# Kernel optimization log

Measured on AMD Instinct MI355X. Metric: run time of the kernel, lower is better.

Reference implementation:

```python
import jax, jax.numpy as jnp
import numpy as np

B, S, H, NH = 8, 4096, 1024, 16
DH = H // NH  # head dim = 64
EPS = 1e-12


def setup_inputs() -> dict:
    key = jax.random.key(0)
    ks = jax.random.split(key, 10)
    sc = 1.0 / np.sqrt(H)
    return {
        "input_tensor": jax.random.normal(ks[0], (B, S, H), dtype=jnp.float32),
        "Wq": jax.random.normal(ks[1], (H, H), dtype=jnp.float32) * sc,
        "bq": jnp.zeros((H,), dtype=jnp.float32),
        "Wk": jax.random.normal(ks[2], (H, H), dtype=jnp.float32) * sc,
        "bk": jnp.zeros((H,), dtype=jnp.float32),
        "Wv": jax.random.normal(ks[3], (H, H), dtype=jnp.float32) * sc,
        "bv": jnp.zeros((H,), dtype=jnp.float32),
        "Wd": jax.random.normal(ks[4], (H, H), dtype=jnp.float32) * sc,
        "bd": jnp.zeros((H,), dtype=jnp.float32),
        "gamma": jnp.ones((H,), dtype=jnp.float32),
        "beta": jnp.zeros((H,), dtype=jnp.float32),
    }


def _heads(x):
    # [B,S,H] -> [B,NH,S,DH]
    return x.reshape(B, S, NH, DH).transpose(0, 2, 1, 3)


def reference(input_tensor, Wq, bq, Wk, bk, Wv, bv, Wd, bd, gamma, beta):
    q = _heads(input_tensor @ Wq + bq)  # [B,NH,S,DH]
    k = _heads(input_tensor @ Wk + bk)
    v = _heads(input_tensor @ Wv + bv)

    eq = jax.nn.elu(q)
    ek = jax.nn.elu(k)
    # L2-normalize per token along the head dim (matches norm over dim=3 of Q
    # and dim=2 of the [B,NH,DH,S]-permuted K in the torch code)
    qn = eq / jnp.linalg.norm(eq, axis=-1, keepdims=True)
    kn = ek / jnp.linalg.norm(ek, axis=-1, keepdims=True)

    kv = jnp.einsum("bhsd,bhse->bhde", kn, v)          # [B,NH,DH,DH]
    ctx = jnp.einsum("bhsd,bhde->bhse", qn, kv) / jnp.sqrt(jnp.float32(DH))
    ctx = ctx.transpose(0, 2, 1, 3).reshape(B, S, H)    # merge heads

    hidden = ctx @ Wd + bd
    x = hidden + input_tensor
    mu = jnp.mean(x, axis=-1, keepdims=True)
    var = jnp.mean(jnp.square(x - mu), axis=-1, keepdims=True)
    return (x - mu) / jnp.sqrt(var + EPS) * gamma + beta
```

## Files before the change

### kernel.cpp

```cpp
#include <hip/hip_runtime.h>
#include <cstdint>
#include <cstddef>

#define B_ 8
#define S_ 4096
#define H_ 1024
#define NH_ 16
#define DH_ 64
#define MTOK 32768

typedef unsigned short u16;
typedef __bf16 bf16x8 __attribute__((ext_vector_type(8)));
typedef u16 u16x8 __attribute__((ext_vector_type(8)));
typedef u16 u16x4 __attribute__((ext_vector_type(4)));
typedef float f32x4 __attribute__((ext_vector_type(4)));

#define DEVFN static __device__ __forceinline__

DEVFN float bf2f(u16 u) {
  union { uint32_t u; float f; } c; c.u = ((uint32_t)u) << 16; return c.f;
}
DEVFN u16 f2bf(float f) {
  union { float f; uint32_t u; } c; c.f = f;
  uint32_t r = c.u + 0x7fffu + ((c.u >> 16) & 1u);
  return (u16)(r >> 16);
}
DEVFN void gload16(const void* g, void* lds_p) {
  __builtin_amdgcn_global_load_lds(
      (const __attribute__((address_space(1))) void*)g,
      (__attribute__((address_space(3))) void*)lds_p, 16, 0, 0);
}

__global__ __launch_bounds__(256) void k_cvt_x(const float* __restrict__ x,
                                               u16* __restrict__ xb) {
  const size_t i = ((size_t)blockIdx.x * 256 + threadIdx.x) * 8;
  f32x4 a = *(const f32x4*)(x + i);
  f32x4 b = *(const f32x4*)(x + i + 4);
  u16x8 o;
#pragma unroll
  for (int j = 0; j < 4; ++j) { o[j] = f2bf(a[j]); o[4 + j] = f2bf(b[j]); }
  *(u16x8*)(xb + i) = o;
}

__global__ __launch_bounds__(256) void k_wt(const float* __restrict__ Wq,
                                            const float* __restrict__ Wk,
                                            const float* __restrict__ Wv,
                                            const float* __restrict__ Wd,
                                            u16* __restrict__ Wt,
                                            u16* __restrict__ Wdt) {
  const int n = blockIdx.x * 256 + threadIdx.x;
  const int kc = blockIdx.y;
  const int g = blockIdx.z;
  const float* W = (g == 0) ? Wq : (g == 1) ? Wk : (g == 2) ? Wv : Wd;
  u16x8 o;
#pragma unroll
  for (int j = 0; j < 8; ++j) o[j] = f2bf(W[(size_t)(kc * 8 + j) * 1024 + n]);
  u16* dst = (g < 3) ? (Wt + ((size_t)(g * 1024 + n)) * 1024 + kc * 8)
                     : (Wdt + (size_t)n * 1024 + kc * 8);
  *(u16x8*)dst = o;
}

template <int EPI>
__global__ __launch_bounds__(512, 2) void k_g(
    const u16* __restrict__ A, const u16* __restrict__ Bt,
    u16* __restrict__ o0, u16* __restrict__ o1, u16* __restrict__ o2,
    const float* __restrict__ b0, const float* __restrict__ b1,
    const float* __restrict__ b2) {
  __shared__ u16 As[2 * 128 * 32];
  __shared__ u16 Bs[2 * 256 * 32];
  const int tid = threadIdx.x;
  const int w = tid >> 6, l = tid & 63;
  const int wm = w >> 2, wn = w & 3;

  const int bid = (int)blockIdx.x;
  const int xcd = bid & 7, c = bid >> 3;
  int bx, by;
  if (EPI == 0) { by = c % 12; bx = xcd * 32 + c / 12; }
  else          { by = c & 3;  bx = xcd * 32 + (c >> 2); }

  const long row0 = (long)bx * 128;
  const long col0 = (long)by * 256;
  const u16* Bt2 = Bt + (EPI == 1 ? ((size_t)(row0 >> 12) << 20) : (size_t)0);

  f32x4 acc[4][4];
#pragma unroll
  for (int i = 0; i < 4; ++i)
#pragma unroll
    for (int j = 0; j < 4; ++j) acc[i][j] = (f32x4){0.f, 0.f, 0.f, 0.f};

  const u16* gA = A + (row0 + (tid >> 2)) * 1024 + (tid & 3) * 8;
  const u16* gB = Bt2 + (col0 + (tid >> 2)) * 1024 + (tid & 3) * 8;
  u16* lA = As + (w * 64) * 8;
  u16* lB = Bs + (w * 64) * 8;

  const int aoff = (wm * 64 + (l & 15)) * 32 + (l >> 4) * 8;
  const int boff = (wn * 64 + (l & 15)) * 32 + (l >> 4) * 8;

  for (int kt = 0; kt < 1024; kt += 64) {
    gload16(gA + kt, lA);
    gload16(gA + kt + 32, lA + 4096);
#pragma unroll
    for (int i = 0; i < 4; ++i) {
      const int go = (i & 1) * 131072 + (i >> 1) * 32 + kt;
      gload16(gB + go, lB + i * 4096);
    }
    __syncthreads();
#pragma unroll
    for (int kh = 0; kh < 2; ++kh) {
      bf16x8 af[4], bfr[4];
#pragma unroll
      for (int mi = 0; mi < 4; ++mi)
        af[mi] = *(const bf16x8*)(As + kh * 4096 + aoff + mi * 512);
#pragma unroll
      for (int ni = 0; ni < 4; ++ni)
        bfr[ni] = *(const bf16x8*)(Bs + kh * 8192 + boff + ni * 512);
#pragma unroll
      for (int mi = 0; mi < 4; ++mi)
#pragma unroll
        for (int ni = 0; ni < 4; ++ni)
          acc[mi][ni] = __builtin_amdgcn_mfma_f32_16x16x32_bf16(
              af[mi], bfr[ni], acc[mi][ni], 0, 0, 0);
    }
    __syncthreads();
  }

  const int rb = (int)row0 + wm * 64 + ((l >> 4) << 2);
  const int cb = (int)col0 + wn * 64 + (l & 15);
  if (EPI == 0) {
    const int seg = (int)(col0 >> 10);
    const int cl = cb & 1023;
    u16* outp = (seg == 0) ? o0 : (seg == 1) ? o1 : o2;
    const float* bias = (seg == 0) ? b0 : (seg == 1) ? b1 : b2;
#pragma unroll
    for (int mi = 0; mi < 4; ++mi)
#pragma unroll
      for (int ni = 0; ni < 4; ++ni) {
        const float bv_ = bias[cl + ni * 16];
#pragma unroll
        for (int r = 0; r < 4; ++r) {
          float v = acc[mi][ni][r] + bv_;
          if (seg < 2) v = v > 0.f ? v : expm1f(v);
          outp[(size_t)(rb + mi * 16 + r) * 1024 + cl + ni * 16] = f2bf(v);
        }
      }
  } else {
#pragma unroll
    for (int mi = 0; mi < 4; ++mi)
#pragma unroll
      for (int ni = 0; ni < 4; ++ni)
#pragma unroll
        for (int r = 0; r < 4; ++r)
          o0[(size_t)(rb + mi * 16 + r) * 1024 + cb + ni * 16] =
              f2bf(acc[mi][ni][r]);
  }
}

__global__ __launch_bounds__(256) void k_qn(u16* __restrict__ eq) {
  const int tid = threadIdx.x, w = tid >> 6, l = tid & 63;
  const long t = (long)blockIdx.x * 4 + w;
  const size_t base = (size_t)t * 1024 + (l >> 2) * 64 + (l & 3) * 16;
  u16x8 a = *(const u16x8*)(eq + base);
  u16x8 b = *(const u16x8*)(eq + base + 8);
  float f[16];
#pragma unroll
  for (int j = 0; j < 8; ++j) { f[j] = bf2f(a[j]); f[8 + j] = bf2f(b[j]); }
  float ss = 0.f;
#pragma unroll
  for (int j = 0; j < 16; ++j) ss += f[j] * f[j];
  ss += __shfl_xor(ss, 1);
  ss += __shfl_xor(ss, 2);
  const float rq = rsqrtf(ss);
  u16x8 oa, ob;
#pragma unroll
  for (int j = 0; j < 8; ++j) { oa[j] = f2bf(f[j] * rq); ob[j] = f2bf(f[8 + j] * rq); }
  *(u16x8*)(eq + base) = oa;
  *(u16x8*)(eq + base + 8) = ob;
}

__global__ __launch_bounds__(256) void k_kv(const u16* __restrict__ ek,
                                            const u16* __restrict__ vv,
                                            float* __restrict__ kvp) {
  __shared__ __align__(16) char lds[69632];
  const int tid = threadIdx.x, w = tid >> 6, l = tid & 63;
  const int bid = blockIdx.x;
  const int sc = bid & 3, h = (bid >> 2) & 15, b = bid >> 6;
  const int tp = l >> 3, dgrp = l & 7;
  char* myk = lds + w * 17408;
  char* myv = myk + 8192;
  const long Tw = (long)b * 4096 + sc * 1024 + w * 256;
  const int d0 = dgrp * 8;

  f32x4 acc[4][4];
#pragma unroll
  for (int i = 0; i < 4; ++i)
#pragma unroll
    for (int j = 0; j < 4; ++j) acc[i][j] = (f32x4){0.f, 0.f, 0.f, 0.f};

  for (int st = 0; st < 4; ++st) {
#pragma unroll
    for (int ro = 0; ro < 4; ++ro) {
      const int tl = ro * 16 + tp * 2;
      const long T = Tw + st * 64 + tl;
      const u16* kp = ek + (size_t)T * 1024 + h * 64 + d0;
      const u16* vp = vv + (size_t)T * 1024 + h * 64 + d0;
      u16x8 k0 = *(const u16x8*)kp, k1 = *(const u16x8*)(kp + 1024);
      u16x8 v0 = *(const u16x8*)vp, v1 = *(const u16x8*)(vp + 1024);
      float f0[8], f1[8], s0 = 0.f, s1 = 0.f;
#pragma unroll
      for (int j = 0; j < 8; ++j) {
        f0[j] = bf2f(k0[j]); s0 += f0[j] * f0[j];
        f1[j] = bf2f(k1[j]); s1 += f1[j] * f1[j];
      }
      s0 += __shfl_xor(s0, 1); s0 += __shfl_xor(s0, 2); s0 += __shfl_xor(s0, 4);
      s1 += __shfl_xor(s1, 1); s1 += __shfl_xor(s1, 2); s1 += __shfl_xor(s1, 4);
      const float r0 = rsqrtf(s0), r1 = rsqrtf(s1);
#pragma unroll
      for (int j = 0; j < 8; ++j) {
        const int d = d0 + j;
        const int sw = (d & 8) ? 32 : 0;
        *(uint32_t*)(myk + d * 128 + ((tl * 2) ^ sw)) =
            (uint32_t)f2bf(f0[j] * r0) | ((uint32_t)f2bf(f1[j] * r1) << 16);
        *(uint32_t*)(myv + d * 128 + ((tl * 2) ^ sw)) =
            (uint32_t)v0[j] | ((uint32_t)v1[j] << 16);
      }
    }
#pragma unroll
    for (int ksl = 0; ksl < 2; ++ksl) {
      const int sb = (ksl * 64 + (l >> 4) * 16) ^ ((l & 8) ? 32 : 0);
      bf16x8 a[4], bb[4];
#pragma unroll
      for (int mf = 0; mf < 4; ++mf)
        a[mf] = *(const bf16x8*)(myk + (mf * 16 + (l & 15)) * 128 + sb);
#pragma unroll
      for (int nf = 0; nf < 4; ++nf)
        bb[nf] = *(const bf16x8*)(myv + (nf * 16 + (l & 15)) * 128 + sb);
#pragma unroll
      for (int mf = 0; mf < 4; ++mf)
#pragma unroll
        for (int nf = 0; nf < 4; ++nf)
          acc[mf][nf] = __builtin_amdgcn_mfma_f32_16x16x32_bf16(
              a[mf], bb[nf], acc[mf][nf], 0, 0, 0);
    }
  }

  __syncthreads();
  float* lf = (float*)(lds + w * 17408);
#pragma unroll
  for (int mf = 0; mf < 4; ++mf)
#pragma unroll
    for (int nf = 0; nf < 4; ++nf)
#pragma unroll
      for (int r = 0; r < 4; ++r)
        lf[(mf * 16 + (l >> 4) * 4 + r) * 68 + nf * 16 + (l & 15)] =
            acc[mf][nf][r];
  __syncthreads();
  float* op = kvp + ((size_t)(sc * 8 + b) * 16 + h) * 4096;
  const float* l0 = (const float*)lds;
  const int dd = tid >> 2, eb = (tid & 3) * 16;
#pragma unroll
  for (int c = 0; c < 4; ++c) {
    f32x4 s = *(const f32x4*)(l0 + dd * 68 + eb + c * 4);
#pragma unroll
    for (int w2 = 1; w2 < 4; ++w2)
      s += *(const f32x4*)(l0 + w2 * 4352 + dd * 68 + eb + c * 4);
    *(f32x4*)(op + tid * 16 + c * 4) = s;
  }
}

__global__ __launch_bounds__(256) void k_m2(const float* __restrict__ kvp,
                                            const u16* __restrict__ Wdt,
                                            u16* __restrict__ M2t) {
  __shared__ __align__(16) u16 lds[12288];
  const int tid = threadIdx.x;
  const int w = tid >> 6, l = tid & 63;
  const int n0 = (int)blockIdx.x * 128, h = (int)blockIdx.y,
            b = (int)blockIdx.z;

#pragma unroll
  for (int g = 0; g < 4; ++g) {
    const int c = g * 256 + tid;
    gload16(Wdt + (size_t)(n0 + (c >> 3)) * 1024 + h * 64 + (c & 7) * 8,
            lds + 4096 + (g * 256 + w * 64) * 8);
  }
  const size_t kvbase = ((size_t)(b * 16 + h)) * 4096;
#pragma unroll
  for (int g = 0; g < 2; ++g) {
    const int c = g * 256 + tid;
    const float* p = kvp + kvbase + (size_t)(c >> 3) * 64 + (c & 7) * 8;
    f32x4 s0 = *(const f32x4*)p;
    f32x4 s1 = *(const f32x4*)(p + 4);
#pragma unroll
    for (int sc = 1; sc < 4; ++sc) {
      s0 += *(const f32x4*)(p + (size_t)sc * 524288);
      s1 += *(const f32x4*)(p + (size_t)sc * 524288 + 4);
    }
    u16x8 o;
#pragma unroll
    for (int j = 0; j < 4; ++j) { o[j] = f2bf(s0[j]); o[4 + j] = f2bf(s1[j]); }
    *(u16x8*)(lds + c * 8) = o;
  }
  __syncthreads();

  f32x4 acc[4][2];
#pragma unroll
  for (int i = 0; i < 4; ++i)
#pragma unroll
    for (int j = 0; j < 2; ++j) acc[i][j] = (f32x4){0.f, 0.f, 0.f, 0.f};

#pragma unroll
  for (int kh = 0; kh < 2; ++kh) {
    bf16x8 a[4], bb[2];
#pragma unroll
    for (int mf = 0; mf < 4; ++mf)
      a[mf] = *(const bf16x8*)(lds + (mf * 16 + (l & 15)) * 64 + kh * 32 +
                               (l >> 4) * 8);
#pragma unroll
    for (int nf = 0; nf < 2; ++nf)
      bb[nf] = *(const bf16x8*)(lds + 4096 +
                                (w * 32 + nf * 16 + (l & 15)) * 64 + kh * 32 +
                                (l >> 4) * 8);
#pragma unroll
    for (int mf = 0; mf < 4; ++mf)
#pragma unroll
      for (int nf = 0; nf < 2; ++nf)
        acc[mf][nf] = __builtin_amdgcn_mfma_f32_16x16x32_bf16(
            a[mf], bb[nf], acc[mf][nf], 0, 0, 0);
  }

  u16* outb = M2t + ((size_t)b << 20) + h * 64;
#pragma unroll
  for (int mf = 0; mf < 4; ++mf)
#pragma unroll
    for (int nf = 0; nf < 2; ++nf) {
      const int col = w * 32 + nf * 16 + (l & 15);
      u16x4 o;
#pragma unroll
      for (int r = 0; r < 4; ++r) o[r] = f2bf(acc[mf][nf][r] * 0.125f);
      *(u16x4*)(outb + (size_t)(n0 + col) * 1024 + mf * 16 + (l >> 4) * 4) = o;
    }
}

__global__ __launch_bounds__(256) void k_ln(const u16* __restrict__ hid,
                                            const u16* __restrict__ xb,
                                            const float* __restrict__ bd,
                                            const float* __restrict__ g,
                                            const float* __restrict__ be,
                                            float* __restrict__ out) {
  const int tid = threadIdx.x, w = tid >> 6, l = tid & 63;
  const size_t base = (size_t)blockIdx.x * 1024 + tid * 4;
  u16x4 h4 = *(const u16x4*)(hid + base);
  u16x4 x4 = *(const u16x4*)(xb + base);
  f32x4 bd4 = *(const f32x4*)(bd + tid * 4);
  float v[4];
#pragma unroll
  for (int j = 0; j < 4; ++j) v[j] = bf2f(h4[j]) + bf2f(x4[j]) + bd4[j];
  float s = v[0] + v[1] + v[2] + v[3];
  float ss = v[0] * v[0] + v[1] * v[1] + v[2] * v[2] + v[3] * v[3];
#pragma unroll
  for (int o = 32; o > 0; o >>= 1) {
    s += __shfl_xor(s, o);
    ss += __shfl_xor(ss, o);
  }
  __shared__ float red[8];
  if (l == 0) { red[w] = s; red[w + 4] = ss; }
  __syncthreads();
  s = red[0] + red[1] + red[2] + red[3];
  ss = red[4] + red[5] + red[6] + red[7];
  const float mu = s * (1.0f / 1024.0f);
  const float var = ss * (1.0f / 1024.0f) - mu * mu;
  const float rstd = rsqrtf(var + 1e-12f);
  f32x4 g4 = *(const f32x4*)(g + tid * 4);
  f32x4 b4 = *(const f32x4*)(be + tid * 4);
  f32x4 o;
#pragma unroll
  for (int j = 0; j < 4; ++j) o[j] = (v[j] - mu) * rstd * g4[j] + b4[j];
  *(f32x4*)(out + base) = o;
}

extern "C" void kernel_launch(void* const* d_in, const int* in_sizes, int n_in,
                              void* d_out, int out_size, void* d_ws,
                              size_t ws_size, hipStream_t stream) {
  const float* X = (const float*)d_in[0];
  const float* Wq = (const float*)d_in[1];
  const float* bq = (const float*)d_in[2];
  const float* Wk = (const float*)d_in[3];
  const float* bk = (const float*)d_in[4];
  const float* Wv = (const float*)d_in[5];
  const float* bv = (const float*)d_in[6];
  const float* Wd = (const float*)d_in[7];
  const float* bd = (const float*)d_in[8];
  const float* gamma = (const float*)d_in[9];
  const float* beta = (const float*)d_in[10];
  float* out = (float*)d_out;

  char* ws = (char*)d_ws;
  u16* Xb = (u16*)(ws);
  u16* Wt = (u16*)(ws + 67108864);
  u16* eq = (u16*)(ws + 73400320);
  u16* ek = (u16*)(ws + 140509184);
  u16* vb = (u16*)(ws + 207618048);
  u16* Wdt = (u16*)(ws + 274726912);
  float* kvp = (float*)(ws + 276824064);
  u16* M2t = (u16*)(ws + 285212672);

  k_cvt_x<<<16384, 256, 0, stream>>>(X, Xb);
  k_wt<<<dim3(4, 128, 4), 256, 0, stream>>>(Wq, Wk, Wv, Wd, Wt, Wdt);
  k_g<0><<<3072, 512, 0, stream>>>(Xb, Wt, eq, ek, vb, bq, bk, bv);
  k_qn<<<8192, 256, 0, stream>>>(eq);
  k_kv<<<512, 256, 0, stream>>>(ek, vb, kvp);
  k_m2<<<dim3(8, 16, 8), 256, 0, stream>>>(kvp, Wdt, M2t);
  k_g<1><<<1024, 512, 0, stream>>>(eq, M2t, ek, nullptr, nullptr, nullptr,
                                   nullptr, nullptr);
  k_ln<<<32768, 256, 0, stream>>>(ek, Xb, bd, gamma, beta, out);
}
```

Baseline: 491.4 us.

## Pre-pack B operand in MFMA fragment order and load it directly to registers

The weight and M2 producers now write the GEMM B operand in a packed layout where each 16-column by 32-k chunk sits in exact MFMA lane order. The GEMM reads B fragments straight from global memory into registers and drops the B shared-memory tile. It also XOR-swizzles the A tile in LDS to cut bank conflicts. This lowers LDS traffic and the LDS footprint, which may allow more occupancy. The cost is that B reuse across the two wave rows now goes through global memory and L2 instead of LDS, and those loads sit in the critical path before the barrier.

```diff
diff --git a/kernel.cpp b/kernel.cpp
--- a/kernel.cpp
+++ b/kernel.cpp
@@ -31,6 +31,7 @@
       (__attribute__((address_space(3))) void*)lds_p, 16, 0, 0);
 }
 
+
 __global__ __launch_bounds__(256) void k_cvt_x(const float* __restrict__ x,
                                                u16* __restrict__ xb) {
   const size_t i = ((size_t)blockIdx.x * 256 + threadIdx.x) * 8;
@@ -46,7 +47,7 @@
                                             const float* __restrict__ Wk,
                                             const float* __restrict__ Wv,
                                             const float* __restrict__ Wd,
-                                            u16* __restrict__ Wt,
+                                            u16* __restrict__ Bp,
                                             u16* __restrict__ Wdt) {
   const int n = blockIdx.x * 256 + threadIdx.x;
   const int kc = blockIdx.y;
@@ -55,19 +56,23 @@
   u16x8 o;
 #pragma unroll
   for (int j = 0; j < 8; ++j) o[j] = f2bf(W[(size_t)(kc * 8 + j) * 1024 + n]);
-  u16* dst = (g < 3) ? (Wt + ((size_t)(g * 1024 + n)) * 1024 + kc * 8)
-                     : (Wdt + (size_t)n * 1024 + kc * 8);
-  *(u16x8*)dst = o;
+  if (g < 3) {
+    const int gn = g * 1024 + n;
+    const int n16 = gn >> 4, ks = kc >> 2;
+    const int lf = (gn & 15) | ((kc & 3) << 4);
+    *(u16x8*)(Bp + ((size_t)(n16 * 32 + ks)) * 512 + lf * 8) = o;
+  } else {
+    *(u16x8*)(Wdt + (size_t)n * 1024 + kc * 8) = o;
+  }
 }
 
 template <int EPI>
 __global__ __launch_bounds__(512, 2) void k_g(
-    const u16* __restrict__ A, const u16* __restrict__ Bt,
+    const u16* __restrict__ A, const u16* __restrict__ Bp,
     u16* __restrict__ o0, u16* __restrict__ o1, u16* __restrict__ o2,
     const float* __restrict__ b0, const float* __restrict__ b1,
     const float* __restrict__ b2) {
   __shared__ u16 As[2 * 128 * 32];
-  __shared__ u16 Bs[2 * 256 * 32];
   const int tid = threadIdx.x;
   const int w = tid >> 6, l = tid & 63;
   const int wm = w >> 2, wn = w & 3;
@@ -80,7 +85,7 @@
 
   const long row0 = (long)bx * 128;
   const long col0 = (long)by * 256;
-  const u16* Bt2 = Bt + (EPI == 1 ? ((size_t)(row0 >> 12) << 20) : (size_t)0);
+  const u16* Bq = Bp + (EPI == 1 ? ((size_t)(row0 >> 12) << 20) : (size_t)0);
 
   f32x4 acc[4][4];
 #pragma unroll
@@ -88,38 +93,39 @@
 #pragma unroll
     for (int j = 0; j < 4; ++j) acc[i][j] = (f32x4){0.f, 0.f, 0.f, 0.f};
 
-  const u16* gA = A + (row0 + (tid >> 2)) * 1024 + (tid & 3) * 8;
-  const u16* gB = Bt2 + (col0 + (tid >> 2)) * 1024 + (tid & 3) * 8;
-  u16* lA = As + (w * 64) * 8;
-  u16* lB = Bs + (w * 64) * 8;
-
-  const int aoff = (wm * 64 + (l & 15)) * 32 + (l >> 4) * 8;
-  const int boff = (wn * 64 + (l & 15)) * 32 + (l >> 4) * 8;
+  const int asl = ((tid & 3) ^ ((tid >> 3) & 3)) * 8;
+  const u16* gA = A + (row0 + (tid >> 2)) * 1024 + asl;
+  u16* lA = As + w * 512;
+
+  const int aoff = (wm * 64 + (l & 15)) * 32 + (((l >> 4) ^ ((l >> 1) & 3)) << 3);
+
+  const int n16b = (int)(col0 >> 4) + wn * 4;
+  const size_t loff = (size_t)l * 8;
 
   for (int kt = 0; kt < 1024; kt += 64) {
     gload16(gA + kt, lA);
     gload16(gA + kt + 32, lA + 4096);
-#pragma unroll
-    for (int i = 0; i < 4; ++i) {
-      const int go = (i & 1) * 131072 + (i >> 1) * 32 + kt;
-      gload16(gB + go, lB + i * 4096);
+    const int ks0 = kt >> 5;
+    bf16x8 bq0[4], bq1[4];
+#pragma unroll
+    for (int nf = 0; nf < 4; ++nf) {
+      const size_t ch = (size_t)((n16b + nf) * 32 + ks0) * 512;
+      bq0[nf] = *(const bf16x8*)(Bq + ch + loff);
+      bq1[nf] = *(const bf16x8*)(Bq + ch + 512 + loff);
     }
     __syncthreads();
 #pragma unroll
     for (int kh = 0; kh < 2; ++kh) {
-      bf16x8 af[4], bfr[4];
+      bf16x8 af[4];
 #pragma unroll
       for (int mi = 0; mi < 4; ++mi)
         af[mi] = *(const bf16x8*)(As + kh * 4096 + aoff + mi * 512);
 #pragma unroll
-      for (int ni = 0; ni < 4; ++ni)
-        bfr[ni] = *(const bf16x8*)(Bs + kh * 8192 + boff + ni * 512);
-#pragma unroll
       for (int mi = 0; mi < 4; ++mi)
 #pragma unroll
-        for (int ni = 0; ni < 4; ++ni)
-          acc[mi][ni] = __builtin_amdgcn_mfma_f32_16x16x32_bf16(
-              af[mi], bfr[ni], acc[mi][ni], 0, 0, 0);
+        for (int nf = 0; nf < 4; ++nf)
+          acc[mi][nf] = __builtin_amdgcn_mfma_f32_16x16x32_bf16(
+              af[mi], kh ? bq1[nf] : bq0[nf], acc[mi][nf], 0, 0, 0);
     }
     __syncthreads();
   }
@@ -269,7 +275,7 @@
 
 __global__ __launch_bounds__(256) void k_m2(const float* __restrict__ kvp,
                                             const u16* __restrict__ Wdt,
-                                            u16* __restrict__ M2t) {
+                                            u16* __restrict__ Bp2) {
   __shared__ __align__(16) u16 lds[12288];
   const int tid = threadIdx.x;
   const int w = tid >> 6, l = tid & 63;
@@ -327,16 +333,20 @@
             a[mf], bb[nf], acc[mf][nf], 0, 0, 0);
   }
 
-  u16* outb = M2t + ((size_t)b << 20) + h * 64;
+  u16* outb = Bp2 + ((size_t)b << 20);
 #pragma unroll
   for (int mf = 0; mf < 4; ++mf)
 #pragma unroll
     for (int nf = 0; nf < 2; ++nf) {
-      const int col = w * 32 + nf * 16 + (l & 15);
+      const int n16 = (n0 >> 4) + w * 2 + nf;
+      const int ks = h * 2 + (mf >> 1);
+      const int oct = ((mf & 1) << 1) | ((l >> 4) >> 1);
+      const int within = ((l >> 4) & 1) * 4;
+      const int lf = (l & 15) | (oct << 4);
       u16x4 o;
 #pragma unroll
       for (int r = 0; r < 4; ++r) o[r] = f2bf(acc[mf][nf][r] * 0.125f);
-      *(u16x4*)(outb + (size_t)(n0 + col) * 1024 + mf * 16 + (l >> 4) * 4) = o;
+      *(u16x4*)(outb + ((size_t)(n16 * 32 + ks)) * 512 + lf * 8 + within) = o;
     }
 }
 
@@ -395,21 +405,21 @@
 
   char* ws = (char*)d_ws;
   u16* Xb = (u16*)(ws);
-  u16* Wt = (u16*)(ws + 67108864);
+  u16* Bp = (u16*)(ws + 67108864);
   u16* eq = (u16*)(ws + 73400320);
   u16* ek = (u16*)(ws + 140509184);
   u16* vb = (u16*)(ws + 207618048);
   u16* Wdt = (u16*)(ws + 274726912);
   float* kvp = (float*)(ws + 276824064);
-  u16* M2t = (u16*)(ws + 285212672);
+  u16* Bp2 = (u16*)(ws + 285212672);
 
   k_cvt_x<<<16384, 256, 0, stream>>>(X, Xb);
-  k_wt<<<dim3(4, 128, 4), 256, 0, stream>>>(Wq, Wk, Wv, Wd, Wt, Wdt);
-  k_g<0><<<3072, 512, 0, stream>>>(Xb, Wt, eq, ek, vb, bq, bk, bv);
+  k_wt<<<dim3(4, 128, 4), 256, 0, stream>>>(Wq, Wk, Wv, Wd, Bp, Wdt);
+  k_g<0><<<3072, 512, 0, stream>>>(Xb, Bp, eq, ek, vb, bq, bk, bv);
   k_qn<<<8192, 256, 0, stream>>>(eq);
   k_kv<<<512, 256, 0, stream>>>(ek, vb, kvp);
-  k_m2<<<dim3(8, 16, 8), 256, 0, stream>>>(kvp, Wdt, M2t);
-  k_g<1><<<1024, 512, 0, stream>>>(eq, M2t, ek, nullptr, nullptr, nullptr,
+  k_m2<<<dim3(8, 16, 8), 256, 0, stream>>>(kvp, Wdt, Bp2);
+  k_g<1><<<1024, 512, 0, stream>>>(eq, Bp2, ek, nullptr, nullptr, nullptr,
                                    nullptr, nullptr);
   k_ln<<<32768, 256, 0, stream>>>(ek, Xb, bd, gamma, beta, out);
 }
```

Result: slower. 509.0 us (+3.6%).
